# Kernel tuning notes

Measured on AMD Instinct MI355X. Metric: run time of the kernel, lower is better.

## Reference

```python
import jax, jax.numpy as jnp
import numpy as np
import math

B, S, DM = 4, 1024, 1024          # batch, seq, d_model
H, D = 16, 64                      # heads, head_size
SE, DF = 512, 512                  # encoder (feature) seq len, feature hidden size
MAXP = 1024                        # max_position_embeddings
LN_EPS = 1e-12


def setup_inputs() -> dict:
    key = jax.random.key(0)
    ks = jax.random.split(key, 20)
    sd = 0.02
    inp = {
        "hidden_states": jax.random.normal(ks[0], (B, S, DM), jnp.float32),
        "attention_mask": jnp.zeros((B, 1, 1, S), jnp.float32),
        "encoder_hidden_states": jax.random.normal(ks[1], (B, SE, DF), jnp.float32),
        # self-attn projections (torch Linear convention: W is [out, in])
        "Wq": jax.random.normal(ks[2], (DM, DM), jnp.float32) * sd,
        "bq": jnp.zeros((DM,), jnp.float32),
        "Wk": jax.random.normal(ks[3], (DM, DM), jnp.float32) * sd,
        "bk": jnp.zeros((DM,), jnp.float32),
        "Wv": jax.random.normal(ks[4], (DM, DM), jnp.float32) * sd,
        "bv": jnp.zeros((DM,), jnp.float32),
        # feature (encoder) projections
        "Wfk": jax.random.normal(ks[5], (DM, DF), jnp.float32) * sd,
        "bfk": jnp.zeros((DM,), jnp.float32),
        "Wfv": jax.random.normal(ks[6], (DM, DF), jnp.float32) * sd,
        "bfv": jnp.zeros((DM,), jnp.float32),
        # relative position embedding table [2*MAXP-1, D]
        "dist_emb": jax.random.normal(ks[7], (2 * MAXP - 1, D), jnp.float32) * sd,
        # RobertaSelfOutput: dense + LayerNorm
        "Wo": jax.random.normal(ks[8], (DM, DM), jnp.float32) * sd,
        "bo": jnp.zeros((DM,), jnp.float32),
        "ln_g": jnp.ones((DM,), jnp.float32),
        "ln_b": jnp.zeros((DM,), jnp.float32),
    }
    return inp


def _split_heads(x):
    b, s, _ = x.shape
    return x.reshape(b, s, H, D).transpose(0, 2, 1, 3)  # [B,H,S,D]


def reference(hidden_states, attention_mask, encoder_hidden_states,
              Wq, bq, Wk, bk, Wv, bv, Wfk, bfk, Wfv, bfv,
              dist_emb, Wo, bo, ln_g, ln_b):
    inv_sqrt_d = 1.0 / math.sqrt(D)

    q = _split_heads(hidden_states @ Wq.T + bq)
    k = _split_heads(hidden_states @ Wk.T + bk)
    v = _split_heads(hidden_states @ Wv.T + bv)

    # raw QK^T scores
    scores = jnp.einsum('bhqd,bhkd->bhqk', q, k)

    # relative_key_query position bias
    pos = jnp.arange(S)
    distance = pos[:, None] - pos[None, :] + (MAXP - 1)  # [S,S] in [0, 2*MAXP-2]
    pe = dist_emb[distance]                               # [S,S,D]
    scores = scores + jnp.einsum('bhld,lrd->bhlr', q, pe) \
                    + jnp.einsum('bhrd,lrd->bhlr', k, pe)

    scores = scores * inv_sqrt_d + attention_mask
    probs = jax.nn.softmax(scores, axis=-1)
    ctx = jnp.einsum('bhqk,bhkd->bhqd', probs, v)  # [B,H,S,D]

    # feature (encoder) cross-attention branch, reusing self-attn queries
    fk = _split_heads(encoder_hidden_states @ Wfk.T + bfk)  # [B,H,SE,D]
    fv = _split_heads(encoder_hidden_states @ Wfv.T + bfv)
    enc_scores = jnp.einsum('bhqd,bhkd->bhqk', q, fk) * inv_sqrt_d
    enc_probs = jax.nn.softmax(enc_scores, axis=-1)
    ctx = ctx + jnp.einsum('bhqk,bhkd->bhqd', enc_probs, fv)

    ctx = ctx.transpose(0, 2, 1, 3).reshape(B, S, DM)  # merge heads

    # RobertaSelfOutput: dense -> residual -> LayerNorm
    y = ctx @ Wo.T + bo + hidden_states
    mu = jnp.mean(y, axis=-1, keepdims=True)
    var = jnp.mean(jnp.square(y - mu), axis=-1, keepdims=True)
    out = (y - mu) * jax.lax.rsqrt(var + LN_EPS) * ln_g + ln_b
    return out
```

## Files before the change

kernel.cpp:

```cpp
#include <hip/hip_runtime.h>


typedef unsigned short u16;
typedef __attribute__((ext_vector_type(8))) short bf16x8;
typedef __attribute__((ext_vector_type(4))) float f32x4;
typedef __attribute__((ext_vector_type(16))) float f32x16;

#define DEV static __device__ __forceinline__

constexpr int H_ = 16, S_ = 1024;

DEV u16 f2bf(float f) {
  unsigned u = __float_as_uint(f);
  unsigned r = (u + 0x7FFFu + ((u >> 16) & 1u)) >> 16;
  return (u16)r;
}
DEV unsigned pack2(float a, float b) {
  return (unsigned)f2bf(a) | ((unsigned)f2bf(b) << 16);
}
DEV float bf2f(u16 u) { return __uint_as_float(((unsigned)u) << 16); }
DEV bf16x8 mk8(unsigned a, unsigned b, unsigned c, unsigned d) {
  union { unsigned u[4]; bf16x8 v; } x;
  x.u[0] = a; x.u[1] = b; x.u[2] = c; x.u[3] = d;
  return x.v;
}
DEV f32x16 zero16() {
  f32x16 z;
#pragma unroll
  for (int i = 0; i < 16; i++) z[i] = 0.f;
  return z;
}
DEV f32x16 mfma32(bf16x8 a, bf16x8 b, f32x16 c) {
  return __builtin_amdgcn_mfma_f32_32x32x16_bf16(a, b, c, 0, 0, 0);
}
DEV f32x4 mfma16(bf16x8 a, bf16x8 b, f32x4 c) {
  return __builtin_amdgcn_mfma_f32_16x16x32_bf16(a, b, c, 0, 0, 0);
}

__global__ __launch_bounds__(256) void k_convert(
    const float* __restrict__ hs, const float* __restrict__ enc,
    const float* __restrict__ wq, const float* __restrict__ wk,
    const float* __restrict__ wv, const float* __restrict__ wo,
    const float* __restrict__ wfk, const float* __restrict__ wfv,
    const float* __restrict__ de,
    u16* __restrict__ o_hs, u16* __restrict__ o_enc, u16* __restrict__ o_wq,
    u16* __restrict__ o_wk, u16* __restrict__ o_wv, u16* __restrict__ o_wo,
    u16* __restrict__ o_wfk, u16* __restrict__ o_wfv, u16* __restrict__ o_e) {
  long i = ((long)blockIdx.x * 256 + threadIdx.x) * 4;
  const float* s; u16* d; long base; bool isE = false;
  if (i < 4194304L)        { s = hs;  d = o_hs;  base = 0L; }
  else if (i < 5242880L)   { s = enc; d = o_enc; base = 4194304L; }
  else if (i < 6291456L)   { s = wq;  d = o_wq;  base = 5242880L; }
  else if (i < 7340032L)   { s = wk;  d = o_wk;  base = 6291456L; }
  else if (i < 8388608L)   { s = wv;  d = o_wv;  base = 7340032L; }
  else if (i < 9437184L)   { s = wo;  d = o_wo;  base = 8388608L; }
  else if (i < 9961472L)   { s = wfk; d = o_wfk; base = 9437184L; }
  else if (i < 10485760L)  { s = wfv; d = o_wfv; base = 9961472L; }
  else                     { s = de;  d = o_e;   base = 10485760L; isE = true; }
  long li = i - base;
  uint2 o;
  if (isE && li >= 131008L) {
    o.x = 0u; o.y = 0u;
  } else {
    float4 v = *(const float4*)(s + li);
    o.x = pack2(v.x, v.y);
    o.y = pack2(v.z, v.w);
  }
  *(uint2*)(d + li) = o;
}

template <int OMODE>
__global__ __launch_bounds__(256) void k_gemm(
    const u16* __restrict__ A, const u16* __restrict__ W,
    const float* __restrict__ bias, void* __restrict__ out,
    const float* __restrict__ resid, int M, int N, int K, int Sdim,
    int sdbits) {
  __shared__ u16 As[128 * 40];
  __shared__ u16 Bs[128 * 40];
  int t = threadIdx.x, w = t >> 6, lane = t & 63;
  int m0 = blockIdx.y * 128, n0 = blockIdx.x * 128;
  int wrow = (w >> 1) * 64, wcol = (w & 1) * 64;
  f32x4 acc[4][4] = {};
  int rs = 32 * w + (lane >> 2);
  int cs = (lane & 3) * 8;
  int nkt = K >> 5;
  for (int kt = 0; kt < nkt; kt++) {
    int k0 = kt << 5;
    bf16x8 ra0 = *(const bf16x8*)(A + (long)(m0 + rs) * K + k0 + cs);
    bf16x8 ra1 = *(const bf16x8*)(A + (long)(m0 + rs + 16) * K + k0 + cs);
    bf16x8 rb0 = *(const bf16x8*)(W + (long)(n0 + rs) * K + k0 + cs);
    bf16x8 rb1 = *(const bf16x8*)(W + (long)(n0 + rs + 16) * K + k0 + cs);
    __syncthreads();
    *(bf16x8*)(As + rs * 40 + cs) = ra0;
    *(bf16x8*)(As + (rs + 16) * 40 + cs) = ra1;
    *(bf16x8*)(Bs + rs * 40 + cs) = rb0;
    *(bf16x8*)(Bs + (rs + 16) * 40 + cs) = rb1;
    __syncthreads();
    bf16x8 af[4], bfr[4];
#pragma unroll
    for (int mi = 0; mi < 4; mi++)
      af[mi] = *(const bf16x8*)(As + (wrow + mi * 16 + (lane & 15)) * 40 +
                                8 * (lane >> 4));
#pragma unroll
    for (int ni = 0; ni < 4; ni++)
      bfr[ni] = *(const bf16x8*)(Bs + (wcol + ni * 16 + (lane & 15)) * 40 +
                                 8 * (lane >> 4));
#pragma unroll
    for (int mi = 0; mi < 4; mi++)
#pragma unroll
      for (int ni = 0; ni < 4; ni++)
        acc[mi][ni] = mfma16(af[mi], bfr[ni], acc[mi][ni]);
  }
#pragma unroll
  for (int mi = 0; mi < 4; mi++) {
#pragma unroll
    for (int ni = 0; ni < 4; ni++) {
      int col = n0 + wcol + ni * 16 + (lane & 15);
      float bcol = bias[col];
#pragma unroll
      for (int e = 0; e < 4; e++) {
        int grow = m0 + wrow + mi * 16 + (lane >> 4) * 4 + e;
        float val = acc[mi][ni][e] + bcol;
        if (OMODE == 2) {
          long idx = (long)grow * N + col;
          ((float*)out)[idx] = val + resid[idx];
        } else {
          int bb = grow >> sdbits, sloc = grow & (Sdim - 1);
          int hh = col >> 6, dd = col & 63;
          long idx;
          if (OMODE == 0)
            idx = ((long)(bb * H_ + hh) * Sdim + sloc) * 64 + dd;
          else
            idx = ((long)(bb * H_ + hh) * 64 + dd) * Sdim + sloc;
          ((u16*)out)[idx] = f2bf(val);
        }
      }
    }
  }
}

template <int NKEYS>
__global__ __launch_bounds__(256) void k_attn_self(
    const u16* __restrict__ qg, const u16* __restrict__ kg,
    const u16* __restrict__ vTg, const u16* __restrict__ eg,
    const float* __restrict__ maskg, float* __restrict__ ctx_f32) {
  __shared__ u16 Ub[4][32 * 64];
  __shared__ u16 Vb[4][32 * 64];
  __shared__ float Sb[4][32];
  int t = threadIdx.x, w = t >> 6, lane = t & 63;
  int lo = lane & 31, hh = lane >> 5;
  int bh = blockIdx.y, bb = bh >> 4, h = bh & 15;
  int l0 = blockIdx.x * 128 + w * 32;
  const u16* qp = qg + (long)bh * S_ * 64;
  const u16* kp = kg + (long)bh * NKEYS * 64;
  const u16* vp = vTg + (long)bh * 64 * NKEYS;
  const float* mp = maskg + bb * S_;
  u16* Up = Ub[w];
  u16* Vp = Vb[w];
  float* Sp = Sb[w];

  bf16x8 qf[4];
#pragma unroll
  for (int kk = 0; kk < 4; kk++)
    qf[kk] = *(const bf16x8*)(qp + (l0 + lo) * 64 + kk * 16 + 8 * hh);

  f32x16 cx0 = zero16(), cx1 = zero16();
  float m_run = -1e30f, s_run = 0.f;
  const float inv = 0.125f;

  for (int r0 = 0; r0 < NKEYS; r0 += 32) {
    bf16x8 kf[4];
#pragma unroll
    for (int kk = 0; kk < 4; kk++)
      kf[kk] = *(const bf16x8*)(kp + (r0 + lo) * 64 + kk * 16 + 8 * hh);
    f32x16 sc = zero16();
#pragma unroll
    for (int kk = 0; kk < 4; kk++) sc = mfma32(kf[kk], qf[kk], sc);

    int mbase = l0 - r0 + 992;
#pragma unroll
    for (int nf = 0; nf < 2; nf++) {
      bf16x8 ef[4];
#pragma unroll
      for (int kk = 0; kk < 4; kk++)
        ef[kk] = *(const bf16x8*)(eg + (long)(mbase + nf * 32 + lo) * 64 +
                                  kk * 16 + 8 * hh);
      f32x16 uu = zero16(), vv = zero16();
#pragma unroll
      for (int kk = 0; kk < 4; kk++) uu = mfma32(qf[kk], ef[kk], uu);
#pragma unroll
      for (int kk = 0; kk < 4; kk++) vv = mfma32(kf[kk], ef[kk], vv);
      int j = nf * 32 + lo;
#pragma unroll
      for (int i = 0; i < 16; i++) {
        int dl = (i & 3) + 8 * (i >> 2) + 4 * hh;
        Up[dl * 64 + j] = f2bf(uu[i]);
        Vp[dl * 64 + j] = f2bf(vv[i]);
      }
    }
    __builtin_amdgcn_s_waitcnt(0);

    float pmax = -1e30f;
#pragma unroll
    for (int i = 0; i < 16; i++) {
      int rr = (i & 3) + 8 * (i >> 2) + 4 * hh;
      int jb = 31 + lo - rr;
      float ubv = bf2f(Up[lo * 64 + jb]);
      float vbv = bf2f(Vp[rr * 64 + jb]);
      float v = (sc[i] + ubv + vbv) * inv + mp[r0 + rr];
      sc[i] = v;
      pmax = fmaxf(pmax, v);
    }
    pmax = fmaxf(pmax, __shfl_xor(pmax, 32));
    float mnew = fmaxf(m_run, pmax);
    float alpha = __expf(m_run - mnew);
    m_run = mnew;
    float tsum = 0.f;
#pragma unroll
    for (int i = 0; i < 16; i++) {
      float p = __expf(sc[i] - mnew);
      sc[i] = p;
      tsum += p;
    }
    tsum += __shfl_xor(tsum, 32);
    s_run = s_run * alpha + tsum;
    if (hh == 0) Sp[lo] = alpha;
    __builtin_amdgcn_s_waitcnt(0);
#pragma unroll
    for (int i = 0; i < 16; i++) {
      float a = Sp[(i & 3) + 8 * (i >> 2) + 4 * hh];
      cx0[i] *= a;
      cx1[i] *= a;
    }
    bf16x8 pA[2];
#pragma unroll
    for (int kk = 0; kk < 2; kk++) {
      unsigned a01 = pack2(sc[8 * kk + 0], sc[8 * kk + 1]);
      unsigned a23 = pack2(sc[8 * kk + 2], sc[8 * kk + 3]);
      unsigned b01 = pack2(sc[8 * kk + 4], sc[8 * kk + 5]);
      unsigned b23 = pack2(sc[8 * kk + 6], sc[8 * kk + 7]);
      unsigned c0a = (unsigned)__shfl((int)a01, lo);
      unsigned c0b = (unsigned)__shfl((int)b01, lo);
      unsigned c1a = (unsigned)__shfl((int)a23, lo);
      unsigned c1b = (unsigned)__shfl((int)b23, lo);
      unsigned c2a = (unsigned)__shfl((int)a01, lo + 32);
      unsigned c2b = (unsigned)__shfl((int)b01, lo + 32);
      unsigned c3a = (unsigned)__shfl((int)a23, lo + 32);
      unsigned c3b = (unsigned)__shfl((int)b23, lo + 32);
      pA[kk] = mk8(hh ? c0b : c0a, hh ? c1b : c1a, hh ? c2b : c2a,
                   hh ? c3b : c3a);
    }
#pragma unroll
    for (int nf = 0; nf < 2; nf++) {
#pragma unroll
      for (int kk = 0; kk < 2; kk++) {
        bf16x8 vf = *(const bf16x8*)(vp + (long)(nf * 32 + lo) * NKEYS + r0 +
                                     kk * 16 + 8 * hh);
        if (nf == 0)
          cx0 = mfma32(pA[kk], vf, cx0);
        else
          cx1 = mfma32(pA[kk], vf, cx1);
      }
    }
  }
  if (hh == 0) Sp[lo] = 1.f / s_run;
  __builtin_amdgcn_s_waitcnt(0);
#pragma unroll
  for (int nf = 0; nf < 2; nf++) {
#pragma unroll
    for (int i = 0; i < 16; i++) {
      int rr = (i & 3) + 8 * (i >> 2) + 4 * hh;
      float val = (nf ? cx1[i] : cx0[i]) * Sp[rr];
      long idx = (long)(bb * S_ + l0 + rr) * 1024 + h * 64 + nf * 32 + lo;
      ctx_f32[idx] = val;
    }
  }
}

template <int NKEYS>
__global__ __launch_bounds__(256) void k_attn_enc(
    const u16* __restrict__ qg, const u16* __restrict__ kg,
    const u16* __restrict__ vTg, const float* __restrict__ ctx_f32,
    u16* __restrict__ ctx_bf) {
  __shared__ float Sb[4][32];
  int t = threadIdx.x, w = t >> 6, lane = t & 63;
  int lo = lane & 31, hh = lane >> 5;
  int bh = blockIdx.y, bb = bh >> 4, h = bh & 15;
  int l0 = blockIdx.x * 128 + w * 32;
  const u16* qp = qg + (long)bh * S_ * 64;
  const u16* kp = kg + (long)bh * NKEYS * 64;
  const u16* vp = vTg + (long)bh * 64 * NKEYS;
  float* Sp = Sb[w];

  bf16x8 qf[4];
#pragma unroll
  for (int kk = 0; kk < 4; kk++)
    qf[kk] = *(const bf16x8*)(qp + (l0 + lo) * 64 + kk * 16 + 8 * hh);

  f32x16 cx0 = zero16(), cx1 = zero16();
  float m_run = -1e30f, s_run = 0.f;
  const float inv = 0.125f;

  for (int r0 = 0; r0 < NKEYS; r0 += 32) {
    bf16x8 kf[4];
#pragma unroll
    for (int kk = 0; kk < 4; kk++)
      kf[kk] = *(const bf16x8*)(kp + (r0 + lo) * 64 + kk * 16 + 8 * hh);
    f32x16 sc = zero16();
#pragma unroll
    for (int kk = 0; kk < 4; kk++) sc = mfma32(kf[kk], qf[kk], sc);

    float pmax = -1e30f;
#pragma unroll
    for (int i = 0; i < 16; i++) {
      float v = sc[i] * inv;
      sc[i] = v;
      pmax = fmaxf(pmax, v);
    }
    pmax = fmaxf(pmax, __shfl_xor(pmax, 32));
    float mnew = fmaxf(m_run, pmax);
    float alpha = __expf(m_run - mnew);
    m_run = mnew;
    float tsum = 0.f;
#pragma unroll
    for (int i = 0; i < 16; i++) {
      float p = __expf(sc[i] - mnew);
      sc[i] = p;
      tsum += p;
    }
    tsum += __shfl_xor(tsum, 32);
    s_run = s_run * alpha + tsum;
    if (hh == 0) Sp[lo] = alpha;
    __builtin_amdgcn_s_waitcnt(0);
#pragma unroll
    for (int i = 0; i < 16; i++) {
      float a = Sp[(i & 3) + 8 * (i >> 2) + 4 * hh];
      cx0[i] *= a;
      cx1[i] *= a;
    }
    bf16x8 pA[2];
#pragma unroll
    for (int kk = 0; kk < 2; kk++) {
      unsigned a01 = pack2(sc[8 * kk + 0], sc[8 * kk + 1]);
      unsigned a23 = pack2(sc[8 * kk + 2], sc[8 * kk + 3]);
      unsigned b01 = pack2(sc[8 * kk + 4], sc[8 * kk + 5]);
      unsigned b23 = pack2(sc[8 * kk + 6], sc[8 * kk + 7]);
      unsigned c0a = (unsigned)__shfl((int)a01, lo);
      unsigned c0b = (unsigned)__shfl((int)b01, lo);
      unsigned c1a = (unsigned)__shfl((int)a23, lo);
      unsigned c1b = (unsigned)__shfl((int)b23, lo);
      unsigned c2a = (unsigned)__shfl((int)a01, lo + 32);
      unsigned c2b = (unsigned)__shfl((int)b01, lo + 32);
      unsigned c3a = (unsigned)__shfl((int)a23, lo + 32);
      unsigned c3b = (unsigned)__shfl((int)b23, lo + 32);
      pA[kk] = mk8(hh ? c0b : c0a, hh ? c1b : c1a, hh ? c2b : c2a,
                   hh ? c3b : c3a);
    }
#pragma unroll
    for (int nf = 0; nf < 2; nf++) {
#pragma unroll
      for (int kk = 0; kk < 2; kk++) {
        bf16x8 vf = *(const bf16x8*)(vp + (long)(nf * 32 + lo) * NKEYS + r0 +
                                     kk * 16 + 8 * hh);
        if (nf == 0)
          cx0 = mfma32(pA[kk], vf, cx0);
        else
          cx1 = mfma32(pA[kk], vf, cx1);
      }
    }
  }
  if (hh == 0) Sp[lo] = 1.f / s_run;
  __builtin_amdgcn_s_waitcnt(0);
#pragma unroll
  for (int nf = 0; nf < 2; nf++) {
#pragma unroll
    for (int i = 0; i < 16; i++) {
      int rr = (i & 3) + 8 * (i >> 2) + 4 * hh;
      float val = (nf ? cx1[i] : cx0[i]) * Sp[rr];
      long idx = (long)(bb * S_ + l0 + rr) * 1024 + h * 64 + nf * 32 + lo;
      ctx_bf[idx] = f2bf(val + ctx_f32[idx]);
    }
  }
}

__global__ __launch_bounds__(256) void k_ln(const float* __restrict__ y,
                                            const float* __restrict__ g,
                                            const float* __restrict__ bta,
                                            float* __restrict__ out) {
  int row = blockIdx.x, t = threadIdx.x;
  const float* yr = y + (long)row * 1024;
  float4 v = *(const float4*)(yr + t * 4);
  float s = v.x + v.y + v.z + v.w;
  float q = v.x * v.x + v.y * v.y + v.z * v.z + v.w * v.w;
#pragma unroll
  for (int off = 1; off < 64; off <<= 1) {
    s += __shfl_xor(s, off);
    q += __shfl_xor(q, off);
  }
  __shared__ float ss[4], qq[4];
  if ((t & 63) == 0) {
    ss[t >> 6] = s;
    qq[t >> 6] = q;
  }
  __syncthreads();
  s = ss[0] + ss[1] + ss[2] + ss[3];
  q = qq[0] + qq[1] + qq[2] + qq[3];
  float mu = s * (1.f / 1024.f);
  float var = q * (1.f / 1024.f) - mu * mu;
  float rinv = rsqrtf(var + 1e-12f);
  float4 gv = *(const float4*)(g + t * 4);
  float4 bv = *(const float4*)(bta + t * 4);
  float4 o;
  o.x = (v.x - mu) * rinv * gv.x + bv.x;
  o.y = (v.y - mu) * rinv * gv.y + bv.y;
  o.z = (v.z - mu) * rinv * gv.z + bv.z;
  o.w = (v.w - mu) * rinv * gv.w + bv.w;
  *(float4*)(out + (long)row * 1024 + t * 4) = o;
}

extern "C" void kernel_launch(void* const* d_in, const int* in_sizes, int n_in,
                              void* d_out, int out_size, void* d_ws,
                              size_t ws_size, hipStream_t stream) {
  (void)in_sizes; (void)n_in; (void)out_size; (void)ws_size;
  const float* hs   = (const float*)d_in[0];
  const float* mask = (const float*)d_in[1];
  const float* enc  = (const float*)d_in[2];
  const float* Wq   = (const float*)d_in[3];
  const float* bq   = (const float*)d_in[4];
  const float* Wk   = (const float*)d_in[5];
  const float* bk   = (const float*)d_in[6];
  const float* Wv   = (const float*)d_in[7];
  const float* bv   = (const float*)d_in[8];
  const float* Wfk  = (const float*)d_in[9];
  const float* bfk  = (const float*)d_in[10];
  const float* Wfv  = (const float*)d_in[11];
  const float* bfv  = (const float*)d_in[12];
  const float* de   = (const float*)d_in[13];
  const float* Wo   = (const float*)d_in[14];
  const float* bo   = (const float*)d_in[15];
  const float* lng  = (const float*)d_in[16];
  const float* lnb  = (const float*)d_in[17];

  char* ws = (char*)d_ws;
  u16* hs_bf  = (u16*)(ws + 0L);
  u16* enc_bf = (u16*)(ws + 8388608L);
  u16* wq_bf  = (u16*)(ws + 10485760L);
  u16* wk_bf  = (u16*)(ws + 12582912L);
  u16* wv_bf  = (u16*)(ws + 14680064L);
  u16* wo_bf  = (u16*)(ws + 16777216L);
  u16* wfk_bf = (u16*)(ws + 18874368L);
  u16* wfv_bf = (u16*)(ws + 19922944L);
  u16* e_bf   = (u16*)(ws + 20971520L);
  u16* q_bf   = (u16*)(ws + 21233664L);
  u16* k_bf   = (u16*)(ws + 29622272L);
  u16* vT_bf  = (u16*)(ws + 38010880L);
  u16* fk_bf  = (u16*)(ws + 46399488L);
  u16* fvT_bf = (u16*)(ws + 50593792L);
  u16* ctx_bf = (u16*)(ws + 54788096L);
  float* ctx1 = (float*)(ws + 0L);
  float* y    = (float*)(ws + 0L);

  k_convert<<<10368, 256, 0, stream>>>(hs, enc, Wq, Wk, Wv, Wo, Wfk, Wfv, de,
                                       hs_bf, enc_bf, wq_bf, wk_bf, wv_bf,
                                       wo_bf, wfk_bf, wfv_bf, e_bf);

  dim3 g4k(8, 32), g2k(8, 16), blk(256);
  k_gemm<0><<<g4k, blk, 0, stream>>>(hs_bf, wq_bf, bq, q_bf, nullptr, 4096,
                                     1024, 1024, 1024, 10);
  k_gemm<0><<<g4k, blk, 0, stream>>>(hs_bf, wk_bf, bk, k_bf, nullptr, 4096,
                                     1024, 1024, 1024, 10);
  k_gemm<1><<<g4k, blk, 0, stream>>>(hs_bf, wv_bf, bv, vT_bf, nullptr, 4096,
                                     1024, 1024, 1024, 10);
  k_gemm<0><<<g2k, blk, 0, stream>>>(enc_bf, wfk_bf, bfk, fk_bf, nullptr, 2048,
                                     1024, 512, 512, 9);
  k_gemm<1><<<g2k, blk, 0, stream>>>(enc_bf, wfv_bf, bfv, fvT_bf, nullptr,
                                     2048, 1024, 512, 512, 9);

  k_attn_self<1024><<<dim3(8, 64), blk, 0, stream>>>(q_bf, k_bf, vT_bf, e_bf,
                                                     mask, ctx1);
  k_attn_enc<512><<<dim3(8, 64), blk, 0, stream>>>(q_bf, fk_bf, fvT_bf, ctx1,
                                                   ctx_bf);

  k_gemm<2><<<g4k, blk, 0, stream>>>(ctx_bf, wo_bf, bo, y, hs, 4096, 1024,
                                     1024, 1024, 10);
  k_ln<<<4096, blk, 0, stream>>>(y, lng, lnb, (float*)d_out);
}
```

Measured before the change: 449.0 us.

## Split self-attention over key halves, fuse projection GEMMs, use direct-to-LDS loads

Self-attention now splits the keys into two halves along a third grid dimension. Each half writes an unnormalized bf16 partial context plus its running max and sum, and the encoder attention kernel merges the halves flash-decoding style. This doubles the number of blocks for the longest kernel. The Q/K/V and feature K/V projections each run as a single launch: the weight matrices are treated as one concatenated N dimension and the output layout is picked per block. The GEMMs drop to 64x128 tiles fed by global_load_lds direct-to-LDS copies, and the full waitcnt fences are replaced with lgkmcnt-only fences. The partial contexts are stored in bf16, which costs some precision and adds extra memory traffic for the merge.

```diff
diff --git a/kernel.cpp b/kernel.cpp
--- a/kernel.cpp
+++ b/kernel.cpp
@@ -36,6 +36,14 @@
 DEV f32x4 mfma16(bf16x8 a, bf16x8 b, f32x4 c) {
   return __builtin_amdgcn_mfma_f32_16x16x32_bf16(a, b, c, 0, 0, 0);
 }
+DEV void gl_lds(const u16* g, u16* l) {
+  __builtin_amdgcn_global_load_lds(
+      (const __attribute__((address_space(1))) unsigned int*)g,
+      (__attribute__((address_space(3))) unsigned int*)l, 16, 0, 0);
+}
+#define LGKM_FENCE()                                   \
+  asm volatile("s_waitcnt lgkmcnt(0)" ::: "memory");   \
+  __builtin_amdgcn_sched_barrier(0)
 
 __global__ __launch_bounds__(256) void k_convert(
     const float* __restrict__ hs, const float* __restrict__ enc,
@@ -69,92 +77,142 @@
   *(uint2*)(d + li) = o;
 }
 
-template <int OMODE>
-__global__ __launch_bounds__(256) void k_gemm(
+__global__ __launch_bounds__(256) void k_gemm_proj(
     const u16* __restrict__ A, const u16* __restrict__ W,
-    const float* __restrict__ bias, void* __restrict__ out,
-    const float* __restrict__ resid, int M, int N, int K, int Sdim,
-    int sdbits) {
-  __shared__ u16 As[128 * 40];
-  __shared__ u16 Bs[128 * 40];
+    const float* __restrict__ b0, const float* __restrict__ b1,
+    const float* __restrict__ b2, u16* __restrict__ d0, u16* __restrict__ d1,
+    u16* __restrict__ d2, int K, int Sdim, int sdbits, int vproj) {
+  __shared__ u16 As[64 * 32];
+  __shared__ u16 Bs[128 * 32];
   int t = threadIdx.x, w = t >> 6, lane = t & 63;
-  int m0 = blockIdx.y * 128, n0 = blockIdx.x * 128;
-  int wrow = (w >> 1) * 64, wcol = (w & 1) * 64;
-  f32x4 acc[4][4] = {};
-  int rs = 32 * w + (lane >> 2);
-  int cs = (lane & 3) * 8;
+  int m0 = blockIdx.y * 64, n0 = blockIdx.x * 128;
+  int wrow = (w >> 1) * 32, wcol = (w & 1) * 64;
+  f32x4 acc[2][4] = {};
+  int srow = lane >> 2;
+  int scol = (lane & 3) * 8;
   int nkt = K >> 5;
   for (int kt = 0; kt < nkt; kt++) {
     int k0 = kt << 5;
-    bf16x8 ra0 = *(const bf16x8*)(A + (long)(m0 + rs) * K + k0 + cs);
-    bf16x8 ra1 = *(const bf16x8*)(A + (long)(m0 + rs + 16) * K + k0 + cs);
-    bf16x8 rb0 = *(const bf16x8*)(W + (long)(n0 + rs) * K + k0 + cs);
-    bf16x8 rb1 = *(const bf16x8*)(W + (long)(n0 + rs + 16) * K + k0 + cs);
     __syncthreads();
-    *(bf16x8*)(As + rs * 40 + cs) = ra0;
-    *(bf16x8*)(As + (rs + 16) * 40 + cs) = ra1;
-    *(bf16x8*)(Bs + rs * 40 + cs) = rb0;
-    *(bf16x8*)(Bs + (rs + 16) * 40 + cs) = rb1;
+    gl_lds(A + (long)(m0 + 16 * w + srow) * K + k0 + scol, As + w * 512);
+    gl_lds(W + (long)(n0 + 32 * w + srow) * K + k0 + scol, Bs + w * 1024);
+    gl_lds(W + (long)(n0 + 32 * w + 16 + srow) * K + k0 + scol,
+           Bs + w * 1024 + 512);
+    asm volatile("s_waitcnt vmcnt(0)" ::: "memory");
     __syncthreads();
-    bf16x8 af[4], bfr[4];
-#pragma unroll
-    for (int mi = 0; mi < 4; mi++)
-      af[mi] = *(const bf16x8*)(As + (wrow + mi * 16 + (lane & 15)) * 40 +
+    bf16x8 af[2], bfr[4];
+#pragma unroll
+    for (int mi = 0; mi < 2; mi++)
+      af[mi] = *(const bf16x8*)(As + (wrow + mi * 16 + (lane & 15)) * 32 +
                                 8 * (lane >> 4));
 #pragma unroll
     for (int ni = 0; ni < 4; ni++)
-      bfr[ni] = *(const bf16x8*)(Bs + (wcol + ni * 16 + (lane & 15)) * 40 +
+      bfr[ni] = *(const bf16x8*)(Bs + (wcol + ni * 16 + (lane & 15)) * 32 +
                                  8 * (lane >> 4));
 #pragma unroll
-    for (int mi = 0; mi < 4; mi++)
+    for (int mi = 0; mi < 2; mi++)
 #pragma unroll
       for (int ni = 0; ni < 4; ni++)
         acc[mi][ni] = mfma16(af[mi], bfr[ni], acc[mi][ni]);
   }
-#pragma unroll
-  for (int mi = 0; mi < 4; mi++) {
-#pragma unroll
-    for (int ni = 0; ni < 4; ni++) {
-      int col = n0 + wcol + ni * 16 + (lane & 15);
-      float bcol = bias[col];
+  int proj = n0 >> 10;
+  const float* bp = proj == 0 ? b0 : (proj == 1 ? b1 : b2);
+  u16* dp = proj == 0 ? d0 : (proj == 1 ? d1 : d2);
+  bool tr = (proj == vproj);
+#pragma unroll
+  for (int ni = 0; ni < 4; ni++) {
+    int col = n0 + wcol + ni * 16 + (lane & 15);
+    int cq = col & 1023;
+    float bcol = bp[cq];
+    int hh = cq >> 6, dd = cq & 63;
+#pragma unroll
+    for (int mi = 0; mi < 2; mi++) {
 #pragma unroll
       for (int e = 0; e < 4; e++) {
         int grow = m0 + wrow + mi * 16 + (lane >> 4) * 4 + e;
-        float val = acc[mi][ni][e] + bcol;
-        if (OMODE == 2) {
-          long idx = (long)grow * N + col;
-          ((float*)out)[idx] = val + resid[idx];
-        } else {
-          int bb = grow >> sdbits, sloc = grow & (Sdim - 1);
-          int hh = col >> 6, dd = col & 63;
-          long idx;
-          if (OMODE == 0)
-            idx = ((long)(bb * H_ + hh) * Sdim + sloc) * 64 + dd;
-          else
-            idx = ((long)(bb * H_ + hh) * 64 + dd) * Sdim + sloc;
-          ((u16*)out)[idx] = f2bf(val);
-        }
+        int bb = grow >> sdbits, sloc = grow & (Sdim - 1);
+        long idx = tr ? ((long)(bb * H_ + hh) * 64 + dd) * Sdim + sloc
+                      : ((long)(bb * H_ + hh) * Sdim + sloc) * 64 + dd;
+        dp[idx] = f2bf(acc[mi][ni][e] + bcol);
       }
     }
   }
 }
 
-template <int NKEYS>
+__global__ __launch_bounds__(256) void k_gemm_out(
+    const u16* __restrict__ A, const u16* __restrict__ W,
+    const float* __restrict__ bias, float* __restrict__ out,
+    const float* __restrict__ resid, int K) {
+  __shared__ u16 As[64 * 32];
+  __shared__ u16 Bs[128 * 32];
+  int t = threadIdx.x, w = t >> 6, lane = t & 63;
+  int m0 = blockIdx.y * 64, n0 = blockIdx.x * 128;
+  int wrow = (w >> 1) * 32, wcol = (w & 1) * 64;
+  f32x4 acc[2][4] = {};
+  int srow = lane >> 2;
+  int scol = (lane & 3) * 8;
+  int nkt = K >> 5;
+  for (int kt = 0; kt < nkt; kt++) {
+    int k0 = kt << 5;
+    __syncthreads();
+    gl_lds(A + (long)(m0 + 16 * w + srow) * K + k0 + scol, As + w * 512);
+    gl_lds(W + (long)(n0 + 32 * w + srow) * K + k0 + scol, Bs + w * 1024);
+    gl_lds(W + (long)(n0 + 32 * w + 16 + srow) * K + k0 + scol,
+           Bs + w * 1024 + 512);
+    asm volatile("s_waitcnt vmcnt(0)" ::: "memory");
+    __syncthreads();
+    bf16x8 af[2], bfr[4];
+#pragma unroll
+    for (int mi = 0; mi < 2; mi++)
+      af[mi] = *(const bf16x8*)(As + (wrow + mi * 16 + (lane & 15)) * 32 +
+                                8 * (lane >> 4));
+#pragma unroll
+    for (int ni = 0; ni < 4; ni++)
+      bfr[ni] = *(const bf16x8*)(Bs + (wcol + ni * 16 + (lane & 15)) * 32 +
+                                 8 * (lane >> 4));
+#pragma unroll
+    for (int mi = 0; mi < 2; mi++)
+#pragma unroll
+      for (int ni = 0; ni < 4; ni++)
+        acc[mi][ni] = mfma16(af[mi], bfr[ni], acc[mi][ni]);
+  }
+#pragma unroll
+  for (int ni = 0; ni < 4; ni++) {
+    int col = n0 + wcol + ni * 16 + (lane & 15);
+    float bcol = bias[col];
+#pragma unroll
+    for (int mi = 0; mi < 2; mi++) {
+#pragma unroll
+      for (int e = 0; e < 4; e++) {
+        int grow = m0 + wrow + mi * 16 + (lane >> 4) * 4 + e;
+        long idx = (long)grow * 1024 + col;
+        out[idx] = acc[mi][ni][e] + bcol + resid[idx];
+      }
+    }
+  }
+}
+
 __global__ __launch_bounds__(256) void k_attn_self(
     const u16* __restrict__ qg, const u16* __restrict__ kg,
     const u16* __restrict__ vTg, const u16* __restrict__ eg,
-    const float* __restrict__ maskg, float* __restrict__ ctx_f32) {
+    const float* __restrict__ maskg, u16* __restrict__ P0,
+    u16* __restrict__ P1, float2* __restrict__ ms0,
+    float2* __restrict__ ms1) {
   __shared__ u16 Ub[4][32 * 64];
   __shared__ u16 Vb[4][32 * 64];
   __shared__ float Sb[4][32];
   int t = threadIdx.x, w = t >> 6, lane = t & 63;
   int lo = lane & 31, hh = lane >> 5;
-  int bh = blockIdx.y, bb = bh >> 4, h = bh & 15;
+  int bh = blockIdx.y;
+  int z = blockIdx.z;
+  int kb = z << 9;
+  u16* Pp = z ? P1 : P0;
+  float2* msp = z ? ms1 : ms0;
   int l0 = blockIdx.x * 128 + w * 32;
   const u16* qp = qg + (long)bh * S_ * 64;
-  const u16* kp = kg + (long)bh * NKEYS * 64;
-  const u16* vp = vTg + (long)bh * 64 * NKEYS;
-  const float* mp = maskg + bb * S_;
+  const u16* kp = kg + (long)bh * S_ * 64;
+  const u16* vp = vTg + (long)bh * 64 * S_;
+  const float* mp = maskg + (bh >> 4) * S_;
   u16* Up = Ub[w];
   u16* Vp = Vb[w];
   float* Sp = Sb[w];
@@ -168,7 +226,7 @@
   float m_run = -1e30f, s_run = 0.f;
   const float inv = 0.125f;
 
-  for (int r0 = 0; r0 < NKEYS; r0 += 32) {
+  for (int r0 = kb; r0 < kb + 512; r0 += 32) {
     bf16x8 kf[4];
 #pragma unroll
     for (int kk = 0; kk < 4; kk++)
@@ -198,7 +256,7 @@
         Vp[dl * 64 + j] = f2bf(vv[i]);
       }
     }
-    __builtin_amdgcn_s_waitcnt(0);
+    LGKM_FENCE();
 
     float pmax = -1e30f;
 #pragma unroll
@@ -225,7 +283,7 @@
     tsum += __shfl_xor(tsum, 32);
     s_run = s_run * alpha + tsum;
     if (hh == 0) Sp[lo] = alpha;
-    __builtin_amdgcn_s_waitcnt(0);
+    LGKM_FENCE();
 #pragma unroll
     for (int i = 0; i < 16; i++) {
       float a = Sp[(i & 3) + 8 * (i >> 2) + 4 * hh];
@@ -254,7 +312,7 @@
     for (int nf = 0; nf < 2; nf++) {
 #pragma unroll
       for (int kk = 0; kk < 2; kk++) {
-        bf16x8 vf = *(const bf16x8*)(vp + (long)(nf * 32 + lo) * NKEYS + r0 +
+        bf16x8 vf = *(const bf16x8*)(vp + (long)(nf * 32 + lo) * S_ + r0 +
                                      kk * 16 + 8 * hh);
         if (nf == 0)
           cx0 = mfma32(pA[kk], vf, cx0);
@@ -263,33 +321,31 @@
       }
     }
   }
-  if (hh == 0) Sp[lo] = 1.f / s_run;
-  __builtin_amdgcn_s_waitcnt(0);
 #pragma unroll
   for (int nf = 0; nf < 2; nf++) {
 #pragma unroll
     for (int i = 0; i < 16; i++) {
       int rr = (i & 3) + 8 * (i >> 2) + 4 * hh;
-      float val = (nf ? cx1[i] : cx0[i]) * Sp[rr];
-      long idx = (long)(bb * S_ + l0 + rr) * 1024 + h * 64 + nf * 32 + lo;
-      ctx_f32[idx] = val;
-    }
-  }
-}
-
-template <int NKEYS>
+      long pidx = ((long)bh * 1024 + l0 + rr) * 64 + nf * 32 + lo;
+      Pp[pidx] = f2bf(nf ? cx1[i] : cx0[i]);
+    }
+  }
+  if (hh == 0) msp[bh * 1024 + l0 + lo] = make_float2(m_run, s_run);
+}
+
 __global__ __launch_bounds__(256) void k_attn_enc(
     const u16* __restrict__ qg, const u16* __restrict__ kg,
-    const u16* __restrict__ vTg, const float* __restrict__ ctx_f32,
-    u16* __restrict__ ctx_bf) {
+    const u16* __restrict__ vTg, const u16* __restrict__ P0,
+    const u16* __restrict__ P1, const float2* __restrict__ ms0,
+    const float2* __restrict__ ms1, u16* __restrict__ ctx_bf) {
   __shared__ float Sb[4][32];
   int t = threadIdx.x, w = t >> 6, lane = t & 63;
   int lo = lane & 31, hh = lane >> 5;
   int bh = blockIdx.y, bb = bh >> 4, h = bh & 15;
   int l0 = blockIdx.x * 128 + w * 32;
   const u16* qp = qg + (long)bh * S_ * 64;
-  const u16* kp = kg + (long)bh * NKEYS * 64;
-  const u16* vp = vTg + (long)bh * 64 * NKEYS;
+  const u16* kp = kg + (long)bh * 512 * 64;
+  const u16* vp = vTg + (long)bh * 64 * 512;
   float* Sp = Sb[w];
 
   bf16x8 qf[4];
@@ -301,7 +357,7 @@
   float m_run = -1e30f, s_run = 0.f;
   const float inv = 0.125f;
 
-  for (int r0 = 0; r0 < NKEYS; r0 += 32) {
+  for (int r0 = 0; r0 < 512; r0 += 32) {
     bf16x8 kf[4];
 #pragma unroll
     for (int kk = 0; kk < 4; kk++)
@@ -331,7 +387,7 @@
     tsum += __shfl_xor(tsum, 32);
     s_run = s_run * alpha + tsum;
     if (hh == 0) Sp[lo] = alpha;
-    __builtin_amdgcn_s_waitcnt(0);
+    LGKM_FENCE();
 #pragma unroll
     for (int i = 0; i < 16; i++) {
       float a = Sp[(i & 3) + 8 * (i >> 2) + 4 * hh];
@@ -360,7 +416,7 @@
     for (int nf = 0; nf < 2; nf++) {
 #pragma unroll
       for (int kk = 0; kk < 2; kk++) {
-        bf16x8 vf = *(const bf16x8*)(vp + (long)(nf * 32 + lo) * NKEYS + r0 +
+        bf16x8 vf = *(const bf16x8*)(vp + (long)(nf * 32 + lo) * 512 + r0 +
                                      kk * 16 + 8 * hh);
         if (nf == 0)
           cx0 = mfma32(pA[kk], vf, cx0);
@@ -370,15 +426,25 @@
     }
   }
   if (hh == 0) Sp[lo] = 1.f / s_run;
-  __builtin_amdgcn_s_waitcnt(0);
-#pragma unroll
-  for (int nf = 0; nf < 2; nf++) {
-#pragma unroll
-    for (int i = 0; i < 16; i++) {
-      int rr = (i & 3) + 8 * (i >> 2) + 4 * hh;
-      float val = (nf ? cx1[i] : cx0[i]) * Sp[rr];
-      long idx = (long)(bb * S_ + l0 + rr) * 1024 + h * 64 + nf * 32 + lo;
-      ctx_bf[idx] = f2bf(val + ctx_f32[idx]);
+  LGKM_FENCE();
+  const float2* m0p = ms0 + (long)bh * 1024;
+  const float2* m1p = ms1 + (long)bh * 1024;
+#pragma unroll
+  for (int i = 0; i < 16; i++) {
+    int rr = (i & 3) + 8 * (i >> 2) + 4 * hh;
+    int l = l0 + rr;
+    float2 a0 = m0p[l], a1 = m1p[l];
+    float Mx = fmaxf(a0.x, a1.x);
+    float w0 = __expf(a0.x - Mx), w1 = __expf(a1.x - Mx);
+    float dn = 1.f / (w0 * a0.y + w1 * a1.y);
+    float sv = Sp[rr];
+#pragma unroll
+    for (int nf = 0; nf < 2; nf++) {
+      long pidx = ((long)bh * 1024 + l) * 64 + nf * 32 + lo;
+      float nself = w0 * bf2f(P0[pidx]) + w1 * bf2f(P1[pidx]);
+      float val = (nf ? cx1[i] : cx0[i]) * sv + nself * dn;
+      ctx_bf[((long)(bb * 1024 + l)) * 1024 + h * 64 + nf * 32 + lo] =
+          f2bf(val);
     }
   }
 }
@@ -457,31 +523,27 @@
   u16* fk_bf  = (u16*)(ws + 46399488L);
   u16* fvT_bf = (u16*)(ws + 50593792L);
   u16* ctx_bf = (u16*)(ws + 54788096L);
-  float* ctx1 = (float*)(ws + 0L);
+  u16* P0     = (u16*)(ws + 0L);
+  u16* P1     = (u16*)(ws + 8388608L);
+  float2* ms0 = (float2*)(ws + 18874368L);
+  float2* ms1 = (float2*)(ws + 19398656L);
   float* y    = (float*)(ws + 0L);
 
   k_convert<<<10368, 256, 0, stream>>>(hs, enc, Wq, Wk, Wv, Wo, Wfk, Wfv, de,
                                        hs_bf, enc_bf, wq_bf, wk_bf, wv_bf,
                                        wo_bf, wfk_bf, wfv_bf, e_bf);
 
-  dim3 g4k(8, 32), g2k(8, 16), blk(256);
-  k_gemm<0><<<g4k, blk, 0, stream>>>(hs_bf, wq_bf, bq, q_bf, nullptr, 4096,
-                                     1024, 1024, 1024, 10);
-  k_gemm<0><<<g4k, blk, 0, stream>>>(hs_bf, wk_bf, bk, k_bf, nullptr, 4096,
-                                     1024, 1024, 1024, 10);
-  k_gemm<1><<<g4k, blk, 0, stream>>>(hs_bf, wv_bf, bv, vT_bf, nullptr, 4096,
-                                     1024, 1024, 1024, 10);
-  k_gemm<0><<<g2k, blk, 0, stream>>>(enc_bf, wfk_bf, bfk, fk_bf, nullptr, 2048,
-                                     1024, 512, 512, 9);
-  k_gemm<1><<<g2k, blk, 0, stream>>>(enc_bf, wfv_bf, bfv, fvT_bf, nullptr,
-                                     2048, 1024, 512, 512, 9);
-
-  k_attn_self<1024><<<dim3(8, 64), blk, 0, stream>>>(q_bf, k_bf, vT_bf, e_bf,
-                                                     mask, ctx1);
-  k_attn_enc<512><<<dim3(8, 64), blk, 0, stream>>>(q_bf, fk_bf, fvT_bf, ctx1,
-                                                   ctx_bf);
-
-  k_gemm<2><<<g4k, blk, 0, stream>>>(ctx_bf, wo_bf, bo, y, hs, 4096, 1024,
-                                     1024, 1024, 10);
+  dim3 blk(256);
+  k_gemm_proj<<<dim3(24, 64), blk, 0, stream>>>(
+      hs_bf, wq_bf, bq, bk, bv, q_bf, k_bf, vT_bf, 1024, 1024, 10, 2);
+  k_gemm_proj<<<dim3(16, 32), blk, 0, stream>>>(
+      enc_bf, wfk_bf, bfk, bfv, bfv, fk_bf, fvT_bf, fvT_bf, 512, 512, 9, 1);
+
+  k_attn_self<<<dim3(8, 64, 2), blk, 0, stream>>>(q_bf, k_bf, vT_bf, e_bf,
+                                                  mask, P0, P1, ms0, ms1);
+  k_attn_enc<<<dim3(8, 64), blk, 0, stream>>>(q_bf, fk_bf, fvT_bf, P0, P1,
+                                              ms0, ms1, ctx_bf);
+
+  k_gemm_out<<<dim3(8, 64), blk, 0, stream>>>(ctx_bf, wo_bf, bo, y, hs, 1024);
   k_ln<<<4096, blk, 0, stream>>>(y, lng, lnb, (float*)d_out);
 }
```

Result: faster. 418.7 us (-6.7%).
